# Optimization experiments

Measured on AMD Instinct MI355X. Metric: run time of the kernel, lower is better.

The kernel has to match this reference:

```python
import jax, jax.numpy as jnp
import numpy as np
from jax.scipy.special import gammaln

# ---- constants matching init_kwargs ----
D = 64            # num_nodes
K = 64            # DiBS latent rank (k = d default)
P = 32            # n_particles
N_MC = 16         # MC graph samples for score-function grad estimator
PROJ = 128        # proj_dims
N = 2048          # observations
H = 5.0           # h_latent (Frobenius squared-exponential kernel bandwidth)
ALPHA = 0.2       # alpha_linear * t  (single SVGD step)
STEP = 0.005      # SVGD step size
ALPHA_MU = 1.0
ALPHA_LAMBD = float(D + 2)
THETA_MU = 0.0
P_EDGE = 4.0 / (D - 1)          # Erdos-Renyi edge prob (~2 expected edges/node)
LATENT_STD = 1.0 / np.sqrt(K)   # DiBS default latent prior std


def bge_log_marginal(g, data, mu0, alpha_mu, alpha_lambd):
    """BGe log marginal likelihood log p(data | G) for 0/1 adjacency g [d,d]."""
    n, d = data.shape
    small_t = alpha_mu * (alpha_lambd - d - 1.0) / (alpha_mu + 1.0)
    xbar = data.mean(0)
    xc = data - xbar
    R = small_t * jnp.eye(d) + xc.T @ xc \
        + (n * alpha_mu / (n + alpha_mu)) * jnp.outer(xbar - mu0, xbar - mu0)

    def masked_slogdet(mask):  # logdet of R restricted to mask-selected rows/cols
        m = jnp.outer(mask, mask)
        return jnp.linalg.slogdet(m * R + (1.0 - m) * jnp.eye(d))[1]

    def node_score(j):
        parents = g[:, j].astype(R.dtype)
        pj = jnp.maximum(parents, (jnp.arange(d) == j).astype(R.dtype))
        l = jnp.sum(parents)
        log_gamma = (0.5 * (jnp.log(alpha_mu) - jnp.log(n + alpha_mu))
                     + gammaln(0.5 * (n + alpha_lambd - d + l + 1.0))
                     - gammaln(0.5 * (alpha_lambd - d + l + 1.0))
                     - 0.5 * n * jnp.log(jnp.pi)
                     + 0.5 * (alpha_lambd - d + 2.0 * l + 1.0) * jnp.log(small_t))
        return (log_gamma
                + 0.5 * (n + alpha_lambd - d + l) * masked_slogdet(parents)
                - 0.5 * (n + alpha_lambd - d + l + 1.0) * masked_slogdet(pj))

    return jnp.sum(jax.vmap(node_score)(jnp.arange(d)))


def _dense(key, fan_in, fan_out):
    return jax.random.normal(key, (fan_in, fan_out), jnp.float32) * 0.05


def setup_inputs() -> dict:
    key = jax.random.key(0)
    ks = jax.random.split(key, 16)
    return {
        "z_gt": jax.random.normal(ks[0], (N, D), jnp.float32),
        "init_particles_z": jax.random.normal(ks[1], (P, D, K, 2), jnp.float32) * LATENT_STD,
        "enc_w0": _dense(ks[2], D * D, 20), "enc_b0": jnp.zeros(20, jnp.float32),
        "enc_w1": _dense(ks[3], 20, D),     "enc_b1": jnp.zeros(D, jnp.float32),
        "enc_w2": _dense(ks[4], D, D),      "enc_b2": jnp.zeros(D, jnp.float32),
        "mu_w0": _dense(ks[5], D, D), "mu_b0": jnp.zeros(D, jnp.float32),
        "mu_w1": _dense(ks[6], D, D), "mu_b1": jnp.zeros(D, jnp.float32),
        "lv_w0": _dense(ks[7], D, D), "lv_b0": jnp.zeros(D, jnp.float32),
        "lv_w1": _dense(ks[8], D, D), "lv_b1": jnp.zeros(D, jnp.float32),
        "dec_w0": _dense(ks[9], D, 10),       "dec_b0": jnp.zeros(10, jnp.float32),
        "dec_w1": _dense(ks[10], 10, PROJ),   "dec_b1": jnp.zeros(PROJ, jnp.float32),
        "dec_w2": _dense(ks[11], PROJ, PROJ), "dec_b2": jnp.zeros(PROJ, jnp.float32),
        "seed": 0,
    }


def reference(z_gt, init_particles_z, enc_w0, enc_b0, enc_w1, enc_b1, enc_w2, enc_b2,
              mu_w0, mu_b0, mu_w1, mu_b1, lv_w0, lv_b0, lv_w1, lv_b1,
              dec_w0, dec_b0, dec_w1, dec_b1, dec_w2, dec_b2, seed):
    key = jax.random.key(seed)
    d = z_gt.shape[1]
    od = 1.0 - jnp.eye(d)
    z = init_particles_z                                   # [P,d,k,2]
    u, v = z[..., 0], z[..., 1]
    scores = jnp.einsum('pik,pjk->pij', u, v)              # [P,d,d]
    probs = jax.nn.sigmoid(ALPHA * scores) * od            # soft graph, zero diag

    # --- score-function estimate of grad_z log E_G[p(data|G)] (DiBS marginal) ---
    key, sk = jax.random.split(key)
    gs = jax.random.bernoulli(sk, probs[:, None], (P, N_MC, d, d)).astype(z.dtype) * od
    mu0_inf = jnp.zeros(d, z.dtype)
    logp = jax.vmap(jax.vmap(
        lambda g: bge_log_marginal(g, z_gt, mu0_inf, 1.0, d + 2.0)))(gs)   # [P,S]
    w = jax.nn.softmax(logp, axis=1)                       # self-normalized weights
    M = ALPHA * (gs - probs[:, None]) * od                 # d log q(G|Z) / d scores
    grad_u = jnp.einsum('ps,psij,pjk->pik', w, M, v)
    grad_v = jnp.einsum('ps,psij,pik->pjk', w, M, u)

    # --- grad of soft-graph ER prior + Gaussian latent prior ---
    logit_pe = jnp.log(P_EDGE) - jnp.log1p(-P_EDGE)
    Mp = ALPHA * probs * (1.0 - probs) * logit_pe * od
    grad_u = grad_u + jnp.einsum('pij,pjk->pik', Mp, v) - u / (LATENT_STD ** 2)
    grad_v = grad_v + jnp.einsum('pij,pik->pjk', Mp, u) - v / (LATENT_STD ** 2)
    grads = jnp.stack([grad_u, grad_v], axis=-1)           # [P,d,k,2]

    # --- one SVGD step with Frobenius squared-exponential kernel ---
    zf = z.reshape(P, -1)
    gf = grads.reshape(P, -1)
    sq = jnp.sum((zf[:, None] - zf[None]) ** 2, -1)
    Kmat = jnp.exp(-sq / H)                                # symmetric [P,P]
    rep = (-2.0 / H) * (Kmat @ zf - zf * Kmat.sum(1, keepdims=True))
    z_new = z + STEP * ((Kmat @ gf + rep) / P).reshape(z.shape)

    # --- hard graphs: particle_to_g_lim (alpha -> inf) ---
    s2 = jnp.einsum('pik,pjk->pij', z_new[..., 0], z_new[..., 1])
    g_hard = (s2 > 0).astype(z.dtype) * od                 # [P,d,d]

    mu0_bge = jnp.full(d, THETA_MU, z.dtype)
    log_p_z_given_g = jax.vmap(
        lambda g: bge_log_marginal(g, z_gt, mu0_bge, ALPHA_MU, ALPHA_LAMBD))(g_hard)

    # --- q(z | G) encoder (batched over particles) ---
    gf2 = g_hard.reshape(g_hard.shape[0], d * d)
    h = jax.nn.relu(gf2 @ enc_w0 + enc_b0)
    h = jax.nn.relu(h @ enc_w1 + enc_b1)
    h = jax.nn.relu(h @ enc_w2 + enc_b2)
    q_mu = jax.nn.relu(h @ mu_w0 + mu_b0) @ mu_w1 + mu_b1
    q_lv = jax.nn.relu(h @ lv_w0 + lv_b0) @ lv_w1 + lv_b1

    key, rk = jax.random.split(key)
    eps = jax.random.normal(rk, q_lv.shape, q_lv.dtype)
    q_z = q_mu + eps * jnp.exp(0.5 * q_lv)                 # reparameterize

    # --- decoder ---
    hdec = jax.nn.relu(q_z @ dec_w0 + dec_b0)
    hdec = jax.nn.relu(hdec @ dec_w1 + dec_b1)
    recons = hdec @ dec_w2 + dec_b2                        # [P, PROJ]

    return recons, log_p_z_given_g, q_z, q_mu, q_lv, g_hard, z_new
```

## Files before the change

### kernel.cpp

```cpp
#include <hip/hip_runtime.h>
#include <stdint.h>
#include <math.h>

typedef unsigned long long u64;
typedef unsigned int u32;
typedef unsigned short u16;

#define C_P 32
#define C_S 16
#define C_D 64
#define C_N 2048

#define R_OFF      0
#define CTAB_OFF   4160
#define KEYS_OFF   4224
#define PROBS_OFF  4232
#define GROW_OFF   135304
#define GCOL_OFF   168072
#define NS_OFF     200840
#define W_OFF      233608
#define GF_OFF     234120
#define KM_OFF     365192
#define ZN_OFF     365704
#define NS2_OFF    496776

#define WL_LIST0 16

#define O_REC   0
#define O_LOGP  4096
#define O_QZ    4128
#define O_QMU   6176
#define O_QLV   8224
#define O_GH    10272
#define O_ZN    141344
#define O_TOTAL 403488

__device__ __forceinline__ void tf2x32(u32 k0, u32 k1, u32 x0, u32 x1,
                                       u32& o0, u32& o1) {
  u32 ks2 = k0 ^ k1 ^ 0x1BD11BDAu;
  x0 += k0; x1 += k1;
#define TFR(r) { x0 += x1; x1 = (x1 << r) | (x1 >> (32 - r)); x1 ^= x0; }
  TFR(13) TFR(15) TFR(26) TFR(6)   x0 += k1;  x1 += ks2 + 1u;
  TFR(17) TFR(29) TFR(16) TFR(24)  x0 += ks2; x1 += k0 + 2u;
  TFR(13) TFR(15) TFR(26) TFR(6)   x0 += k0;  x1 += k1 + 3u;
  TFR(17) TFR(29) TFR(16) TFR(24)  x0 += k1;  x1 += ks2 + 4u;
  TFR(13) TFR(15) TFR(26) TFR(6)   x0 += ks2; x1 += k0 + 5u;
#undef TFR
  o0 = x0; o1 = x1;
}

__device__ __forceinline__ double d_erfinv(double x) {
  double w = -log1p(-x * x);
  double p;
  if (w < 5.0) {
    w -= 2.5;
    p = 2.81022636e-08;
    p = 3.43273939e-07  + p * w;
    p = -3.5233877e-06  + p * w;
    p = -4.39150654e-06 + p * w;
    p = 0.00021858087   + p * w;
    p = -0.00125372503  + p * w;
    p = -0.00417768164  + p * w;
    p = 0.246640727     + p * w;
    p = 1.50140941      + p * w;
  } else {
    w = sqrt(w) - 3.0;
    p = -0.000200214257;
    p = 0.000100950558  + p * w;
    p = 0.00134934322   + p * w;
    p = -0.00367342844  + p * w;
    p = 0.00573950773   + p * w;
    p = -0.0076224613   + p * w;
    p = 0.00943887047   + p * w;
    p = 1.00167406      + p * w;
    p = 2.83297682      + p * w;
  }
  return p * x;
}

__global__ void k_R(const float* x, double* ws, const int* seedp) {
  __shared__ double pS[8][64], pX[8][64];
  __shared__ double xbar[64];
  int j = blockIdx.x, t = threadIdx.x;
  int i = t & 63, c = t >> 6;
  if (j == 0) {
    if (t < 64) {
      double l = (double)t;
      ws[CTAB_OFF + t] = -0.5 * log(2049.0)
                       + lgamma(0.5 * (2051.0 + l))
                       - lgamma(0.5 * (3.0 + l))
                       - 1024.0 * log(3.14159265358979323846)
                       + 0.5 * (2.0 * l + 3.0) * log(0.5);
    }
    if (t < 4) ((u32*)(ws + GF_OFF))[t] = 0;
    if (t == 0) {
      u32 kk0 = 0u, kk1 = (u32)seedp[0];
      u32 a0, a1, s0, s1, r0, r1, d0, d1;
      tf2x32(kk0, kk1, 0u, 0u, a0, a1);
      tf2x32(kk0, kk1, 0u, 1u, s0, s1);
      tf2x32(a0, a1, 0u, 0u, d0, d1); (void)d0; (void)d1;
      tf2x32(a0, a1, 0u, 1u, r0, r1);
      u32* keys = (u32*)(ws + KEYS_OFF);
      keys[0] = s0; keys[1] = s1; keys[2] = r0; keys[3] = r1;
    }
  }
  double sx = 0.0, sxx = 0.0;
  for (int n = c * 256; n < (c + 1) * 256; n++) {
    double xi = (double)x[n * 64 + i];
    double xj = (double)x[n * 64 + j];
    sx += xi; sxx += xi * xj;
  }
  pS[c][i] = sx; pX[c][i] = sxx;
  __syncthreads();
  if (t < 64) {
    double S = 0.0, X = 0.0;
    for (int cc = 0; cc < 8; cc++) { S += pS[cc][i]; X += pX[cc][i]; }
    xbar[i] = S / 2048.0;
    pX[0][i] = X;
  }
  __syncthreads();
  if (t < 64) {
    double xbi = xbar[i], xbj = xbar[j];
    double s = pX[0][i] - 2048.0 * xbi * xbj + (2048.0 / 2049.0) * xbi * xbj;
    if (i == j) s += 0.5;
    ((float*)(ws + R_OFF))[i * 64 + j] = (float)s;
  }
}

__global__ __launch_bounds__(64) void k_probs(const float* z, double* ws) {
  float* probs = (float*)(ws + PROBS_OFF);
  int b = blockIdx.x; int p = b >> 6, i = b & 63;
  int j = threadIdx.x;
  __shared__ float V[64 * 65];
  __shared__ float us[64];
  int k = j;
  us[k] = z[((p * 64 + i) * 64 + k) * 2 + 0];
  for (int jj = 0; jj < 64; jj++)
    V[jj * 65 + k] = z[((p * 64 + jj) * 64 + k) * 2 + 1];
  __syncthreads();
  float s = 0.f;
  for (int kk = 0; kk < 64; kk++)
    s += us[kk] * V[j * 65 + kk];
  float pr = (i == j) ? 0.f : 1.f / (1.f + expf(-0.2f * s));
  probs[(p * 64 + i) * 64 + j] = pr;
}

__global__ void k_sample(double* ws) {
  const float* probs = (const float*)(ws + PROBS_OFF);
  const u32* keys = (const u32*)(ws + KEYS_OFF);
  u64* grow = (u64*)(ws + GROW_OFF);
  u64* gcol = (u64*)(ws + GCOL_OFF);
  u32* wl = (u32*)(ws + GF_OFF);
  int ps = blockIdx.x;
  int p = ps >> 4;
  int j = threadIdx.x;
  u32 k0 = keys[0], k1 = keys[1];
  u64 colmask = 0;
  for (int i = 0; i < 64; i++) {
    u32 lin = (u32)(ps * 4096 + i * 64 + j);
    u32 o0, o1; tf2x32(k0, k1, 0u, lin, o0, o1);
    u32 bits = o0 ^ o1;
    float f = __uint_as_float((bits >> 9) | 0x3f800000u) - 1.0f;
    bool bit = (f < probs[(p * 64 + i) * 64 + j]);
    u64 rm = __ballot(bit);
    if (j == 0) grow[ps * 64 + i] = rm;
    if (bit) colmask |= (1ull << i);
  }
  gcol[ps * 64 + j] = colmask;
  int m = (int)__popcll(colmask) + 1;
  int tier = (m <= 34) ? 0 : ((m <= 40) ? 1 : 2);
#pragma unroll
  for (int t = 0; t < 3; t++) {
    u64 b = __ballot(tier == t);
    if (tier == t) {
      int leader = (int)__builtin_ctzll(b);
      u32 off = (u32)__popcll(b & ((1ull << j) - 1ull));
      u32 base = 0;
      if (j == leader) base = atomicAdd(&wl[t], (u32)__popcll(b));
      base = (u32)__shfl((int)base, leader, 64);
      wl[WL_LIST0 + t * 32768 + base + off] = (u32)(ps * 64 + j);
    }
  }
}

__device__ __forceinline__ float rdlane(float x, int l) {
  return __uint_as_float(__builtin_amdgcn_readlane(__float_as_uint(x), (u32)l));
}

template<int MMAX>
__global__ __launch_bounds__(256) void k_chol_tier(const float* Rf, const double* ctab,
                                                   const u64* masks, double* nodescore,
                                                   const u32* wl, int tier) {
  __shared__ int idx[4][64];
  int w = threadIdx.x >> 6;
  int lane = threadIdx.x & 63;
  u32 cnt = wl[tier];
  const u32* list = wl + WL_LIST0 + tier * 32768;
  for (u32 ti = blockIdx.x * 4 + w; ti < cnt; ti += gridDim.x * 4) {
    int task = (int)list[ti];
    int j = task & 63;
    u64 mask = masks[task];
    int P = (int)__popcll(mask);
    int m = P + 1;
    idx[w][lane] = 0;
    __builtin_amdgcn_wave_barrier();
    u64 below = mask & ((1ull << lane) - 1ull);
    if ((mask >> lane) & 1ull) idx[w][(int)__popcll(below)] = lane;
    if (lane == 0) idx[w][P] = j;
    __builtin_amdgcn_wave_barrier();
    int myrow = idx[w][lane];
    float v[MMAX];
#pragma unroll
    for (int c = 0; c < MMAX; c++)
      v[c] = Rf[idx[w][c] * 64 + myrow];
    float mypiv = 1.0f, lastd = 1.0f;
#pragma unroll
    for (int k = 0; k < MMAX; k++) {
      if (k < m) {
        float dk = rdlane(v[k], k);
        if (lane == k) mypiv = dk;
        lastd = dk;
        float ns = -v[k] * __builtin_amdgcn_rcpf(dk);
#pragma unroll
        for (int b = k + 1; b < MMAX; b++)
          v[b] += ns * rdlane(v[k], b);
      }
    }
    float lv = (lane < m) ? __logf(mypiv) : 0.f;
    for (int off = 32; off > 0; off >>= 1) lv += __shfl_down(lv, off, 64);
    if (lane == 0) {
      float loglast = __logf(lastd);
      double l = (double)P;
      nodescore[task] = ctab[P]
                      - 0.5 * (2050.0 + l) * (double)loglast
                      - 0.5 * (double)lv;
    }
    __builtin_amdgcn_wave_barrier();
  }
}

__global__ __launch_bounds__(64) void k_chol_heavy(const float* Rf, const double* ctab,
                                                   const u64* masks, double* nodescore,
                                                   const u32* wl) {
  __shared__ float T[2080];
  __shared__ int idx[64];
  int lane = threadIdx.x;
  u32 cnt = wl[2];
  const u32* list = wl + WL_LIST0 + 2 * 32768;
  for (u32 ii = blockIdx.x; ii < cnt; ii += gridDim.x) {
    __syncthreads();
    int task = (int)list[ii];
    int j = task & 63;
    u64 mask = masks[task];
    int P = (int)__popcll(mask);
    int m = P + 1;
    u64 below = mask & ((1ull << lane) - 1ull);
    if ((mask >> lane) & 1ull) idx[(int)__popcll(below)] = lane;
    if (lane == 0) idx[P] = j;
    __syncthreads();
    int trLane = (lane * (lane + 1)) >> 1;
    if (lane < m) {
      int cidx = idx[lane];
      int tr = 0;
      for (int r = 0; r < m; r++) {
        if (lane <= r) T[tr + lane] = Rf[idx[r] * 64 + cidx];
        tr += r + 1;
      }
    }
    __syncthreads();
    float mypiv = 1.0f, lastd = 1.0f;
    float v[40];
#pragma unroll
    for (int c = 0; c < 40; c++)
      v[c] = T[trLane + c];
#pragma unroll
    for (int k = 0; k < 40; k++) {
      if (k < m) {
        float dk = rdlane(v[k], k);
        if (lane == k) mypiv = dk;
        lastd = dk;
        float ns = -v[k] * __builtin_amdgcn_rcpf(dk);
#pragma unroll
        for (int b = k + 1; b < 40; b++)
          v[b] += ns * rdlane(v[k], b);
      }
    }
    if (m > 40) {
      for (int b = 40; b < m; b++) {
        float acc = 0.f;
#pragma unroll
        for (int k = 0; k < 40; k++) {
          float dk = rdlane(v[k], k);
          float abk = rdlane(v[k], b);
          acc += v[k] * abk * __builtin_amdgcn_rcpf(dk);
        }
        if (lane >= b) T[trLane + b] -= acc;
      }
      __syncthreads();
      for (int k = 40; k < m; k++) {
        float dk = T[((k * (k + 1)) >> 1) + k];
        if (lane == k) mypiv = dk;
        lastd = dk;
        float sk = T[trLane + k] * __builtin_amdgcn_rcpf(dk);
        for (int b = k + 1; b < m; b++) {
          float abk = T[((b * (b + 1)) >> 1) + k];
          if (lane >= b) T[trLane + b] -= sk * abk;
        }
        __syncthreads();
      }
    }
    double vv = (lane < m) ? log((double)mypiv) : 0.0;
    for (int off = 32; off > 0; off >>= 1) vv += __shfl_down(vv, off, 64);
    if (lane == 0) {
      double logB = vv;
      double logA = logB - log((double)lastd);
      double l = (double)P;
      nodescore[task] = ctab[P]
                      + 0.5 * (2050.0 + l) * logA
                      - 0.5 * (2051.0 + l) * logB;
    }
  }
}

template<bool TRANSPOSE>
__global__ __launch_bounds__(64) void k_chol(const float* Rf, const double* ctab,
                                             const u64* masks, double* nodescore) {
  __shared__ float T[2080];
  __shared__ int idx[64];
  int task = blockIdx.x;
  int j = task & 63;
  int lane = threadIdx.x;
  u64 mask;
  if (TRANSPOSE) {
    int p = task >> 6;
    u64 rm = masks[p * 64 + lane];
    mask = __ballot((rm >> j) & 1ull);
  } else {
    mask = masks[task];
  }
  int P = (int)__popcll(mask);
  int m = P + 1;
  u64 below = mask & ((1ull << lane) - 1ull);
  if ((mask >> lane) & 1ull) idx[(int)__popcll(below)] = lane;
  if (lane == 0) idx[P] = j;
  __syncthreads();
  int trLane = (lane * (lane + 1)) >> 1;
  if (lane < m) {
    int cidx = idx[lane];
    int tr = 0;
    for (int r = 0; r < m; r++) {
      if (lane <= r) T[tr + lane] = Rf[idx[r] * 64 + cidx];
      tr += r + 1;
    }
  }
  __syncthreads();
  float mypiv = 1.0f, lastd = 1.0f;
  float v[40];
#pragma unroll
  for (int c = 0; c < 40; c++)
    v[c] = T[trLane + c];
#pragma unroll
  for (int k = 0; k < 40; k++) {
    if (k < m) {
      float dk = rdlane(v[k], k);
      if (lane == k) mypiv = dk;
      lastd = dk;
      float ns = -v[k] * __builtin_amdgcn_rcpf(dk);
#pragma unroll
      for (int b = k + 1; b < 40; b++)
        v[b] += ns * rdlane(v[k], b);
    }
  }
  if (m > 40) {
    for (int b = 40; b < m; b++) {
      float acc = 0.f;
#pragma unroll
      for (int k = 0; k < 40; k++) {
        float dk = rdlane(v[k], k);
        float abk = rdlane(v[k], b);
        acc += v[k] * abk * __builtin_amdgcn_rcpf(dk);
      }
      if (lane >= b) T[trLane + b] -= acc;
    }
    __syncthreads();
    for (int k = 40; k < m; k++) {
      float dk = T[((k * (k + 1)) >> 1) + k];
      if (lane == k) mypiv = dk;
      lastd = dk;
      float sk = T[trLane + k] * __builtin_amdgcn_rcpf(dk);
      for (int b = k + 1; b < m; b++) {
        float abk = T[((b * (b + 1)) >> 1) + k];
        if (lane >= b) T[trLane + b] -= sk * abk;
      }
      __syncthreads();
    }
  }
  double vv = (lane < m) ? log((double)mypiv) : 0.0;
  for (int off = 32; off > 0; off >>= 1) vv += __shfl_down(vv, off, 64);
  if (lane == 0) {
    double logB = vv;
    double logA = logB - log((double)lastd);
    double l = (double)P;
    nodescore[task] = ctab[P]
                    + 0.5 * (2050.0 + l) * logA
                    - 0.5 * (2051.0 + l) * logB;
  }
}

__global__ void k_logpw(const double* ns, double* w) {
  int p = blockIdx.x, t = threadIdx.x;
  __shared__ double part[64];
  int s = t & 15, c = t >> 4;
  double acc = 0.0;
  for (int j = c * 16; j < (c + 1) * 16; j++)
    acc += ns[(p * 16 + s) * 64 + j];
  part[t] = acc;
  __syncthreads();
  if (t < 16) part[t] = part[t] + part[t + 16] + part[t + 32] + part[t + 48];
  __syncthreads();
  if (t == 0) {
    double m = part[0];
    for (int s2 = 1; s2 < 16; s2++) m = fmax(m, part[s2]);
    double e[16], sum = 0.0;
    for (int s2 = 0; s2 < 16; s2++) { e[s2] = exp(part[s2] - m); sum += e[s2]; }
    for (int s2 = 0; s2 < 16; s2++) w[p * 16 + s2] = e[s2] / sum;
  }
}

__global__ void k_grad(double* ws, const float* z) {
  const float* probs = (const float*)(ws + PROBS_OFF);
  const double* w = ws + W_OFF;
  const u64* grow = (const u64*)(ws + GROW_OFF);
  const u64* gcol = (const u64*)(ws + GCOL_OFF);
  float* gf = (float*)(ws + GF_OFF);
  const float LOGIT = -2.6903717578966254f;
  int bb = blockIdx.x;
  int k = threadIdx.x;
  __shared__ float acc[64];
  if (bb < 2048) {
    int p = bb >> 6, i = bb & 63;
    float gb = 0.f, wsum = 0.f;
    for (int s = 0; s < 16; s++) {
      float wv = (float)w[p * 16 + s];
      wsum += wv;
      gb += wv * (float)((grow[(p * 16 + s) * 64 + i] >> k) & 1ull);
    }
    float pr = probs[(p * 64 + i) * 64 + k];
    float od = (i == k) ? 0.f : 1.f;
    acc[k] = (0.2f * (gb - pr * wsum) + 0.2f * pr * (1.f - pr) * LOGIT) * od;
    __syncthreads();
    float s = 0.f;
    for (int j = 0; j < 64; j++)
      s += acc[j] * z[((p * 64 + j) * 64 + k) * 2 + 1];
    s -= 64.f * z[((p * 64 + i) * 64 + k) * 2 + 0];
    gf[p * 8192 + (i * 64 + k) * 2 + 0] = s;
  } else if (bb < 4096) {
    int b = bb - 2048;
    int p = b >> 6, j = b & 63;
    float gb = 0.f, wsum = 0.f;
    for (int s = 0; s < 16; s++) {
      float wv = (float)w[p * 16 + s];
      wsum += wv;
      gb += wv * (float)((gcol[(p * 16 + s) * 64 + j] >> k) & 1ull);
    }
    float pr = probs[(p * 64 + k) * 64 + j];
    float od = (k == j) ? 0.f : 1.f;
    acc[k] = (0.2f * (gb - pr * wsum) + 0.2f * pr * (1.f - pr) * LOGIT) * od;
    __syncthreads();
    float s = 0.f;
    for (int i = 0; i < 64; i++)
      s += acc[i] * z[((p * 64 + i) * 64 + k) * 2 + 0];
    s -= 64.f * z[((p * 64 + j) * 64 + k) * 2 + 1];
    gf[p * 8192 + (j * 64 + k) * 2 + 1] = s;
  } else {
    float* Km = (float*)(ws + KM_OFF);
    int b = bb - 4096;
    int a = b >> 5, b2 = b & 31;
    float accf = 0.f;
    for (int d0 = k; d0 < 8192; d0 += 64) {
      float diff = z[a * 8192 + d0] - z[b2 * 8192 + d0];
      accf += diff * diff;
    }
    for (int off = 32; off > 0; off >>= 1) accf += __shfl_down(accf, off, 64);
    if (k == 0) Km[a * 32 + b2] = expf(-accf / 5.0f);
  }
}

__global__ void k_znew(const float* z, double* ws, float* out) {
  const float* Km = (const float*)(ws + KM_OFF);
  const float* gf = (const float*)(ws + GF_OFF);
  float* zn = (float*)(ws + ZN_OFF);
  int gid = blockIdx.x * 64 + threadIdx.x;
  int p = gid >> 13, t = gid & 8191;
  float zp = z[p * 8192 + t];
  float accg = 0.f, accz = 0.f, ks = 0.f;
  for (int b = 0; b < 32; b++) {
    float kv = Km[p * 32 + b];
    accg += kv * gf[b * 8192 + t];
    accz += kv * z[b * 8192 + t];
    ks += kv;
  }
  float rep = -0.4f * (accz - zp * ks);
  float v = zp + 0.005f * ((accg + rep) / 32.f);
  zn[p * 8192 + t] = v;
  out[O_ZN + p * 8192 + t] = v;
}

__global__ __launch_bounds__(64) void k_s2col(double* ws, float* out) {
  const float* zn = (const float*)(ws + ZN_OFF);
  u64* grow2 = (u64*)(ws + NS_OFF);
  int b = blockIdx.x; int p = b >> 6, i = b & 63;
  int j = threadIdx.x;
  __shared__ float V[64 * 65];
  __shared__ float us[64];
  int k = j;
  us[k] = zn[p * 8192 + (i * 64 + k) * 2 + 0];
  for (int jj = 0; jj < 64; jj++)
    V[jj * 65 + k] = zn[p * 8192 + (jj * 64 + k) * 2 + 1];
  __syncthreads();
  float s = 0.f;
  for (int kk = 0; kk < 64; kk++)
    s += us[kk] * V[j * 65 + kk];
  bool bit = (i != j) && (s > 0.0f);
  out[O_GH + (p * 64 + i) * 64 + j] = bit ? 1.0f : 0.0f;
  u64 m = __ballot(bit);
  if (j == 0) grow2[p * 64 + i] = m;
}

__global__ __launch_bounds__(256) void k_mlp(double* ws, float* out, const double* ns2,
    const float* ew0, const float* eb0, const float* ew1, const float* eb1,
    const float* ew2, const float* eb2,
    const float* mw0, const float* mb0, const float* mw1, const float* mb1,
    const float* lw0, const float* lb0, const float* lw1, const float* lb1,
    const float* dw0, const float* db0, const float* dw1, const float* db1,
    const float* dw2, const float* db2) {
  int p = blockIdx.x, t = threadIdx.x;
  int w = t >> 6, lane = t & 63;
  const u64* grow2 = (const u64*)(ws + NS_OFF);
  const u32* keys = (const u32*)(ws + KEYS_OFF);
  __shared__ float pt[4][64];
  __shared__ float e0p[4][20];
  __shared__ float h0[20], h1[64], h2[64], hm[64], hl[64];
  __shared__ float qmu[64], qlv[64], qz[64], h3[10], h4[128];

  if (w == 0) {
    double vv = ns2[p * 64 + lane];
    for (int off = 32; off > 0; off >>= 1) vv += __shfl_down(vv, off, 64);
    if (lane == 0) out[O_LOGP + p] = (float)vv;
  }

  {
    int i = t >> 2;
    int jb = (t & 3) * 16;
    u32 m16 = (u32)((grow2[p * 64 + i] >> jb) & 0xFFFFull);
    float acc[20];
#pragma unroll
    for (int o = 0; o < 20; o++) acc[o] = 0.f;
    const float* wbase = ew0 + (size_t)(t * 16) * 20;
#pragma unroll
    for (int q = 0; q < 16; q++) {
      if ((m16 >> q) & 1u) {
        const float* wr = wbase + q * 20;
#pragma unroll
        for (int o = 0; o < 20; o++) acc[o] += wr[o];
      }
    }
#pragma unroll
    for (int o = 0; o < 20; o++) {
      float v = acc[o];
      for (int off = 32; off > 0; off >>= 1) v += __shfl_down(v, off, 64);
      if (lane == 0) e0p[w][o] = v;
    }
  }
  __syncthreads();
  if (t < 20)
    h0[t] = fmaxf(eb0[t] + e0p[0][t] + e0p[1][t] + e0p[2][t] + e0p[3][t], 0.f);
  __syncthreads();

  {
    float s = 0.f;
#pragma unroll
    for (int q = 0; q < 5; q++) s += h0[w * 5 + q] * ew1[(w * 5 + q) * 64 + lane];
    pt[w][lane] = s;
  }
  __syncthreads();
  if (w == 0)
    h1[lane] = fmaxf(eb1[lane] + pt[0][lane] + pt[1][lane] + pt[2][lane] + pt[3][lane], 0.f);
  __syncthreads();

  {
    float s = 0.f;
#pragma unroll
    for (int q = 0; q < 16; q++) s += h1[w * 16 + q] * ew2[(w * 16 + q) * 64 + lane];
    pt[w][lane] = s;
  }
  __syncthreads();
  if (w == 0)
    h2[lane] = fmaxf(eb2[lane] + pt[0][lane] + pt[1][lane] + pt[2][lane] + pt[3][lane], 0.f);
  __syncthreads();

  {
    const float* W = (w < 2) ? mw0 : lw0;
    int qb = (w & 1) * 32;
    float s = 0.f;
#pragma unroll
    for (int q = 0; q < 32; q++) s += h2[qb + q] * W[(qb + q) * 64 + lane];
    pt[w][lane] = s;
  }
  __syncthreads();
  if (w == 0) hm[lane] = fmaxf(mb0[lane] + pt[0][lane] + pt[1][lane], 0.f);
  if (w == 1) hl[lane] = fmaxf(lb0[lane] + pt[2][lane] + pt[3][lane], 0.f);
  __syncthreads();

  {
    const float* W = (w < 2) ? mw1 : lw1;
    const float* src = (w < 2) ? hm : hl;
    int qb = (w & 1) * 32;
    float s = 0.f;
#pragma unroll
    for (int q = 0; q < 32; q++) s += src[qb + q] * W[(qb + q) * 64 + lane];
    pt[w][lane] = s;
  }
  __syncthreads();
  if (w == 0) qmu[lane] = mb1[lane] + pt[0][lane] + pt[1][lane];
  if (w == 1) qlv[lane] = lb1[lane] + pt[2][lane] + pt[3][lane];
  __syncthreads();

  if (w == 0) {
    u32 o0, o1;
    tf2x32(keys[2], keys[3], 0u, (u32)(p * 64 + lane), o0, o1);
    u32 bits = o0 ^ o1;
    float f = __uint_as_float((bits >> 9) | 0x3f800000u) - 1.0f;
    float LOF = __uint_as_float(0xBF7FFFFFu);
    float uu = fmaxf(LOF, f * 2.0f + LOF);
    float eps = (float)(1.4142135623730951 * d_erfinv((double)uu));
    float qzv = qmu[lane] + eps * expf(0.5f * qlv[lane]);
    qz[lane] = qzv;
    out[O_QZ  + p * 64 + lane] = qzv;
    out[O_QMU + p * 64 + lane] = qmu[lane];
    out[O_QLV + p * 64 + lane] = qlv[lane];
  }
  __syncthreads();

  {
    float s = 0.f;
    if (lane < 10) {
#pragma unroll
      for (int q = 0; q < 16; q++) s += qz[w * 16 + q] * dw0[(w * 16 + q) * 10 + lane];
    }
    pt[w][lane] = s;
  }
  __syncthreads();
  if (w == 0 && lane < 10)
    h3[lane] = fmaxf(db0[lane] + pt[0][lane] + pt[1][lane] + pt[2][lane] + pt[3][lane], 0.f);
  __syncthreads();

  {
    int o = (w >> 1) * 64 + lane;
    int qb = (w & 1) * 5;
    float s = 0.f;
#pragma unroll
    for (int q = 0; q < 5; q++) s += h3[qb + q] * dw1[(qb + q) * 128 + o];
    pt[w][lane] = s;
  }
  __syncthreads();
  if (w == 0) h4[lane]      = fmaxf(db1[lane]      + pt[0][lane] + pt[1][lane], 0.f);
  if (w == 1) h4[64 + lane] = fmaxf(db1[64 + lane] + pt[2][lane] + pt[3][lane], 0.f);
  __syncthreads();

  {
    int o = (w >> 1) * 64 + lane;
    int qb = (w & 1) * 64;
    float s = 0.f;
#pragma unroll
    for (int q = 0; q < 64; q++) s += h4[qb + q] * dw2[(qb + q) * 128 + o];
    pt[w][lane] = s;
  }
  __syncthreads();
  if (w == 0) out[O_REC + p * 128 + lane]      = db2[lane]      + pt[0][lane] + pt[1][lane];
  if (w == 1) out[O_REC + p * 128 + 64 + lane] = db2[64 + lane] + pt[2][lane] + pt[3][lane];
}

extern "C" void kernel_launch(void* const* d_in, const int* in_sizes, int n_in,
                              void* d_out, int out_size, void* d_ws, size_t ws_size,
                              hipStream_t stream) {
  (void)in_sizes; (void)n_in; (void)out_size; (void)ws_size;
  const float* z_gt = (const float*)d_in[0];
  const float* z0   = (const float*)d_in[1];
  const float* ew0 = (const float*)d_in[2];  const float* eb0 = (const float*)d_in[3];
  const float* ew1 = (const float*)d_in[4];  const float* eb1 = (const float*)d_in[5];
  const float* ew2 = (const float*)d_in[6];  const float* eb2 = (const float*)d_in[7];
  const float* mw0 = (const float*)d_in[8];  const float* mb0 = (const float*)d_in[9];
  const float* mw1 = (const float*)d_in[10]; const float* mb1 = (const float*)d_in[11];
  const float* lw0 = (const float*)d_in[12]; const float* lb0 = (const float*)d_in[13];
  const float* lw1 = (const float*)d_in[14]; const float* lb1 = (const float*)d_in[15];
  const float* dw0 = (const float*)d_in[16]; const float* db0 = (const float*)d_in[17];
  const float* dw1 = (const float*)d_in[18]; const float* db1 = (const float*)d_in[19];
  const float* dw2 = (const float*)d_in[20]; const float* db2 = (const float*)d_in[21];
  const int* seed = (const int*)d_in[22];
  double* ws = (double*)d_ws;
  float* out = (float*)d_out;
  const float* Rf = (const float*)(ws + R_OFF);
  const u32* wl = (const u32*)(ws + GF_OFF);

  k_R<<<64, 512, 0, stream>>>(z_gt, ws, seed);
  k_probs<<<C_P * C_D, 64, 0, stream>>>(z0, ws);
  k_sample<<<C_P * C_S, 64, 0, stream>>>(ws);
  k_chol_tier<34><<<6144, 256, 0, stream>>>(Rf, ws + CTAB_OFF,
      (const u64*)(ws + GCOL_OFF), ws + NS_OFF, wl, 0);
  k_chol_tier<40><<<2560, 256, 0, stream>>>(Rf, ws + CTAB_OFF,
      (const u64*)(ws + GCOL_OFF), ws + NS_OFF, wl, 1);
  k_chol_heavy<<<1024, 64, 0, stream>>>(Rf, ws + CTAB_OFF,
      (const u64*)(ws + GCOL_OFF), ws + NS_OFF, wl);
  k_logpw<<<C_P, 64, 0, stream>>>(ws + NS_OFF, ws + W_OFF);
  k_grad<<<2 * C_P * C_D + C_P * C_P, 64, 0, stream>>>(ws, z0);
  k_znew<<<(C_P * 8192) / 64, 64, 0, stream>>>(z0, ws, out);
  k_s2col<<<C_P * C_D, 64, 0, stream>>>(ws, out);
  k_chol<true><<<C_P * C_D, 64, 0, stream>>>(Rf, ws + CTAB_OFF,
      (const u64*)(ws + NS_OFF), ws + NS2_OFF);
  k_mlp<<<C_P, 256, 0, stream>>>(ws, out, ws + NS2_OFF,
      ew0, eb0, ew1, eb1, ew2, eb2,
      mw0, mb0, mw1, mb1, lw0, lb0, lw1, lb1,
      dw0, db0, dw1, db1, dw2, db2);
}
```

Baseline: 348.4 us.

## Merge Cholesky tier kernels into one launch with finer size tiers

Replaces the three separate Cholesky launches (two register tiers plus a heavy kernel) with one combined kernel. It splits the work into five size tiers (29/32/35/40/heavy) and assigns each a fixed block range, so smaller tiles use fewer registers and the tiers run concurrently instead of serially. The lgamma constant table is now built from a Stirling approximation plus a prefix-sum recurrence, the heavy path swaps block syncs for wave barriers, and the encoder's first layer uses branchless float4 loads. The combined kernel shares one shared-memory footprint and one launch bound across tiers, which may reduce occupancy for the small tiers, and the fixed block split can leave tiers unbalanced.

```diff
diff --git a/kernel.cpp b/kernel.cpp
--- a/kernel.cpp
+++ b/kernel.cpp
@@ -25,6 +25,17 @@
 #define NS2_OFF    496776
 
 #define WL_LIST0 16
+
+#define TB0 1792
+#define TB1 2304
+#define TB2 2176
+#define TB3 1728
+#define HBLK 384
+#define S1 (TB0)
+#define S2 (TB0+TB1)
+#define S3 (TB0+TB1+TB2)
+#define SH (TB0+TB1+TB2+TB3)
+#define NBLK_ALL (SH+HBLK)
 
 #define O_REC   0
 #define O_LOGP  4096
@@ -78,6 +89,14 @@
   return p * x;
 }
 
+__device__ __forceinline__ double stirl(double z) {
+  double zi = 1.0 / z;
+  double zi2 = zi * zi;
+  double s = (z - 0.5) * log(z) - z + 0.9189385332046727;
+  s += zi * (1.0 / 12.0 - zi2 * (1.0 / 360.0 - zi2 * (1.0 / 1260.0)));
+  return s;
+}
+
 __global__ void k_R(const float* x, double* ws, const int* seedp) {
   __shared__ double pS[8][64], pX[8][64];
   __shared__ double xbar[64];
@@ -85,14 +104,24 @@
   int i = t & 63, c = t >> 6;
   if (j == 0) {
     if (t < 64) {
-      double l = (double)t;
-      ws[CTAB_OFF + t] = -0.5 * log(2049.0)
-                       + lgamma(0.5 * (2051.0 + l))
-                       - lgamma(0.5 * (3.0 + l))
-                       - 1024.0 * log(3.14159265358979323846)
-                       + 0.5 * (2.0 * l + 3.0) * log(0.5);
-    }
-    if (t < 4) ((u32*)(ws + GF_OFF))[t] = 0;
+      int l = t;
+      double term = (l >= 2) ? log((2049.0 + (double)l) / (4.0 * (1.0 + (double)l)))
+                             : 0.0;
+      double v = term;
+#pragma unroll
+      for (int off = 2; off <= 32; off <<= 1) {
+        double o = __shfl_up(v, off, 64);
+        if (l >= off) v += o;
+      }
+      const double LOG_HALF = -0.6931471805599453;
+      double c0 = -0.5 * log(2049.0)
+                - 1024.0 * log(3.14159265358979323846);
+      double seed = (l & 1)
+        ? c0 + stirl(1026.0) + 2.5 * LOG_HALF
+        : c0 + stirl(1025.5) + 0.12078223763524522235 + 1.5 * LOG_HALF;
+      ws[CTAB_OFF + l] = seed + v;
+    }
+    if (t < 8) ((u32*)(ws + GF_OFF))[t] = 0;
     if (t == 0) {
       u32 kk0 = 0u, kk1 = (u32)seedp[0];
       u32 a0, a1, s0, s1, r0, r1, d0, d1;
@@ -168,9 +197,9 @@
   }
   gcol[ps * 64 + j] = colmask;
   int m = (int)__popcll(colmask) + 1;
-  int tier = (m <= 34) ? 0 : ((m <= 40) ? 1 : 2);
-#pragma unroll
-  for (int t = 0; t < 3; t++) {
+  int tier = (m <= 29) ? 0 : (m <= 32) ? 1 : (m <= 35) ? 2 : (m <= 40) ? 3 : 4;
+#pragma unroll
+  for (int t = 0; t < 5; t++) {
     u64 b = __ballot(tier == t);
     if (tier == t) {
       int leader = (int)__builtin_ctzll(b);
@@ -188,15 +217,15 @@
 }
 
 template<int MMAX>
-__global__ __launch_bounds__(256) void k_chol_tier(const float* Rf, const double* ctab,
-                                                   const u64* masks, double* nodescore,
-                                                   const u32* wl, int tier) {
-  __shared__ int idx[4][64];
+__device__ __forceinline__ void tier_body(const float* Rf, const double* ctab,
+                                          const u64* masks, double* nodescore,
+                                          const u32* wl, int tier,
+                                          u32 brel, u32 nb, int (*idx)[64]) {
   int w = threadIdx.x >> 6;
   int lane = threadIdx.x & 63;
   u32 cnt = wl[tier];
   const u32* list = wl + WL_LIST0 + tier * 32768;
-  for (u32 ti = blockIdx.x * 4 + w; ti < cnt; ti += gridDim.x * 4) {
+  for (u32 ti = brel * 4 + (u32)w; ti < cnt; ti += nb * 4) {
     int task = (int)list[ti];
     int j = task & 63;
     u64 mask = masks[task];
@@ -213,42 +242,43 @@
 #pragma unroll
     for (int c = 0; c < MMAX; c++)
       v[c] = Rf[idx[w][c] * 64 + myrow];
-    float mypiv = 1.0f, lastd = 1.0f;
+    float mypiv = 1.0f;
 #pragma unroll
     for (int k = 0; k < MMAX; k++) {
       if (k < m) {
         float dk = rdlane(v[k], k);
         if (lane == k) mypiv = dk;
-        lastd = dk;
         float ns = -v[k] * __builtin_amdgcn_rcpf(dk);
 #pragma unroll
         for (int b = k + 1; b < MMAX; b++)
           v[b] += ns * rdlane(v[k], b);
       }
     }
+    float lastd = __shfl(mypiv, P, 64);
     float lv = (lane < m) ? __logf(mypiv) : 0.f;
     for (int off = 32; off > 0; off >>= 1) lv += __shfl_down(lv, off, 64);
     if (lane == 0) {
-      float loglast = __logf(lastd);
       double l = (double)P;
       nodescore[task] = ctab[P]
-                      - 0.5 * (2050.0 + l) * (double)loglast
+                      - 0.5 * (2050.0 + l) * (double)__logf(lastd)
                       - 0.5 * (double)lv;
     }
     __builtin_amdgcn_wave_barrier();
   }
 }
 
-__global__ __launch_bounds__(64) void k_chol_heavy(const float* Rf, const double* ctab,
-                                                   const u64* masks, double* nodescore,
-                                                   const u32* wl) {
-  __shared__ float T[2080];
-  __shared__ int idx[64];
+#define WB() __builtin_amdgcn_wave_barrier()
+
+__device__ void heavy_body(const float* Rf, const double* ctab,
+                           const u64* masks, double* nodescore,
+                           const u32* wl, u32 brel, u32 nb,
+                           float* T, int* idx) {
+  if (threadIdx.x >= 64) return;
   int lane = threadIdx.x;
-  u32 cnt = wl[2];
-  const u32* list = wl + WL_LIST0 + 2 * 32768;
-  for (u32 ii = blockIdx.x; ii < cnt; ii += gridDim.x) {
-    __syncthreads();
+  u32 cnt = wl[4];
+  const u32* list = wl + WL_LIST0 + 4 * 32768;
+  for (u32 ii = brel; ii < cnt; ii += nb) {
+    WB();
     int task = (int)list[ii];
     int j = task & 63;
     u64 mask = masks[task];
@@ -257,7 +287,7 @@
     u64 below = mask & ((1ull << lane) - 1ull);
     if ((mask >> lane) & 1ull) idx[(int)__popcll(below)] = lane;
     if (lane == 0) idx[P] = j;
-    __syncthreads();
+    WB();
     int trLane = (lane * (lane + 1)) >> 1;
     if (lane < m) {
       int cidx = idx[lane];
@@ -267,7 +297,7 @@
         tr += r + 1;
       }
     }
-    __syncthreads();
+    WB();
     float mypiv = 1.0f, lastd = 1.0f;
     float v[40];
 #pragma unroll
@@ -296,7 +326,7 @@
         }
         if (lane >= b) T[trLane + b] -= acc;
       }
-      __syncthreads();
+      WB();
       for (int k = 40; k < m; k++) {
         float dk = T[((k * (k + 1)) >> 1) + k];
         if (lane == k) mypiv = dk;
@@ -306,7 +336,7 @@
           float abk = T[((b * (b + 1)) >> 1) + k];
           if (lane >= b) T[trLane + b] -= sk * abk;
         }
-        __syncthreads();
+        WB();
       }
     }
     double vv = (lane < m) ? log((double)mypiv) : 0.0;
@@ -320,6 +350,20 @@
                       - 0.5 * (2051.0 + l) * logB;
     }
   }
+}
+
+__global__ __launch_bounds__(256) void k_chol_all(const float* Rf, const double* ctab,
+                                                  const u64* masks, double* nodescore,
+                                                  const u32* wl) {
+  __shared__ int idx4[4][64];
+  __shared__ float T[2080];
+  __shared__ int idxh[64];
+  u32 b = blockIdx.x;
+  if (b < TB0)     tier_body<29>(Rf, ctab, masks, nodescore, wl, 0, b,      TB0, idx4);
+  else if (b < S2) tier_body<32>(Rf, ctab, masks, nodescore, wl, 1, b - S1, TB1, idx4);
+  else if (b < S3) tier_body<35>(Rf, ctab, masks, nodescore, wl, 2, b - S2, TB2, idx4);
+  else if (b < SH) tier_body<40>(Rf, ctab, masks, nodescore, wl, 3, b - S3, TB3, idx4);
+  else             heavy_body(Rf, ctab, masks, nodescore, wl, b - SH, HBLK, T, idxh);
 }
 
 template<bool TRANSPOSE>
@@ -556,14 +600,17 @@
     float acc[20];
 #pragma unroll
     for (int o = 0; o < 20; o++) acc[o] = 0.f;
-    const float* wbase = ew0 + (size_t)(t * 16) * 20;
+    const float4* wb = (const float4*)(ew0 + (size_t)(t * 16) * 20);
 #pragma unroll
     for (int q = 0; q < 16; q++) {
-      if ((m16 >> q) & 1u) {
-        const float* wr = wbase + q * 20;
-#pragma unroll
-        for (int o = 0; o < 20; o++) acc[o] += wr[o];
-      }
+      float mq = (float)((m16 >> q) & 1u);
+      float4 r0 = wb[q * 5 + 0], r1 = wb[q * 5 + 1], r2 = wb[q * 5 + 2];
+      float4 r3 = wb[q * 5 + 3], r4 = wb[q * 5 + 4];
+      acc[0]  += mq * r0.x; acc[1]  += mq * r0.y; acc[2]  += mq * r0.z; acc[3]  += mq * r0.w;
+      acc[4]  += mq * r1.x; acc[5]  += mq * r1.y; acc[6]  += mq * r1.z; acc[7]  += mq * r1.w;
+      acc[8]  += mq * r2.x; acc[9]  += mq * r2.y; acc[10] += mq * r2.z; acc[11] += mq * r2.w;
+      acc[12] += mq * r3.x; acc[13] += mq * r3.y; acc[14] += mq * r3.z; acc[15] += mq * r3.w;
+      acc[16] += mq * r4.x; acc[17] += mq * r4.y; acc[18] += mq * r4.z; acc[19] += mq * r4.w;
     }
 #pragma unroll
     for (int o = 0; o < 20; o++) {
@@ -706,11 +753,7 @@
   k_R<<<64, 512, 0, stream>>>(z_gt, ws, seed);
   k_probs<<<C_P * C_D, 64, 0, stream>>>(z0, ws);
   k_sample<<<C_P * C_S, 64, 0, stream>>>(ws);
-  k_chol_tier<34><<<6144, 256, 0, stream>>>(Rf, ws + CTAB_OFF,
-      (const u64*)(ws + GCOL_OFF), ws + NS_OFF, wl, 0);
-  k_chol_tier<40><<<2560, 256, 0, stream>>>(Rf, ws + CTAB_OFF,
-      (const u64*)(ws + GCOL_OFF), ws + NS_OFF, wl, 1);
-  k_chol_heavy<<<1024, 64, 0, stream>>>(Rf, ws + CTAB_OFF,
+  k_chol_all<<<NBLK_ALL, 256, 0, stream>>>(Rf, ws + CTAB_OFF,
       (const u64*)(ws + GCOL_OFF), ws + NS_OFF, wl);
   k_logpw<<<C_P, 64, 0, stream>>>(ws + NS_OFF, ws + W_OFF);
   k_grad<<<2 * C_P * C_D + C_P * C_P, 64, 0, stream>>>(ws, z0);
```

New measurement: 364.6 us. 4.7% more time.
